# Performance work log

Measured on AMD Instinct MI355X. Metric: run time of the kernel, lower is better.

The kernel has to match this reference:

```python
import jax, jax.numpy as jnp
import numpy as np

BASIS_SIZE = 256          # levels of the bitfield code
R_MAX = 1.0               # quantization range for normalized weights
QMAX = BASIS_SIZE // 2 - 1  # 127 -> symmetric int8-style grid
EPS = 1e-8


def setup_inputs() -> dict:
    key = jax.random.key(0)
    kx, kw, kb = jax.random.split(key, 3)
    B, S, D_IN, D_OUT = 4, 2048, 4096, 4096
    x = jax.random.normal(kx, (B, S, D_IN), dtype=jnp.float32)
    W = jax.random.normal(kw, (D_OUT, D_IN), dtype=jnp.float32)
    bias = jax.random.normal(kb, (D_OUT,), dtype=jnp.float32)
    return {"x": x, "W": W, "bias": bias}


def _bitfield_dequant_weight(W):
    # per-output-row L2 norm (p=2, dim=1 in torch)
    weight_norms = jnp.sqrt(jnp.sum(W * W, axis=1))          # [out]
    W_normalized = W / (weight_norms[:, None] + EPS)          # rows ~unit norm
    # bitfield encode/decode: uniform symmetric quantization to BASIS_SIZE
    # levels in [-R_MAX, R_MAX]
    scale = R_MAX / QMAX
    Wq = jnp.round(jnp.clip(W_normalized, -R_MAX, R_MAX) / scale) * scale
    return Wq, weight_norms


def reference(x, W, bias):
    Wq, weight_norms = _bitfield_dequant_weight(W)
    B, S, D_IN = x.shape
    x2 = x.reshape(-1, D_IN)                                  # [B*S, in]
    # bitfield matmul on normalized weights
    out_norm = jnp.einsum('nd,od->no', x2, Wq)                # [B*S, out]
    # denormalize (restore row norms) + bias epilogue
    out = out_norm * weight_norms
    out = out.reshape(B, S, -1) + bias
    return out
```

## Files before the change

kernel.cpp:

```cpp
#include <hip/hip_runtime.h>

typedef __attribute__((ext_vector_type(4))) int i32x4;
typedef __attribute__((ext_vector_type(16))) int i32x16;
typedef unsigned long long ull;

#define D_IN  4096
#define D_OUT 4096
#define M_TOT 8192

__device__ __forceinline__ int pack4(float a, float b, float c, float d, float s) {
  int q0 = (int)rintf(a * s) & 255;
  int q1 = (int)rintf(b * s) & 255;
  int q2 = (int)rintf(c * s) & 255;
  int q3 = (int)rintf(d * s) & 255;
  return q0 | (q1 << 8) | (q2 << 16) | (q3 << 24);
}

__global__ void quant_pack_kernel(const float* __restrict__ x, const float* __restrict__ W,
                                  char* __restrict__ XP, char* __restrict__ WP,
                                  float* __restrict__ sx, float* __restrict__ sn) {
  __shared__ float  redf[4];
  __shared__ double redd[4];
  __shared__ float  bc;
  const int bid = blockIdx.x, t = threadIdx.x;

  if (bid < M_TOT) {
    const int r = bid;
    const float4* xr = (const float4*)(x + (size_t)r * D_IN);
    float4 v[4];
    float mx = 0.f;
#pragma unroll
    for (int q = 0; q < 4; q++) {
      v[q] = xr[t * 4 + q];
      mx = fmaxf(mx, fmaxf(fmaxf(fabsf(v[q].x), fabsf(v[q].y)),
                           fmaxf(fabsf(v[q].z), fabsf(v[q].w))));
    }
#pragma unroll
    for (int off = 32; off; off >>= 1) mx = fmaxf(mx, __shfl_xor(mx, off));
    if ((t & 63) == 0) redf[t >> 6] = mx;
    __syncthreads();
    if (t == 0) {
      float m = fmaxf(fmaxf(redf[0], redf[1]), fmaxf(redf[2], redf[3]));
      bc = m;
      sx[r] = m * (1.0f / 127.0f);
    }
    __syncthreads();
    const float inv = 127.0f / bc;
    int4 o;
    o.x = pack4(v[0].x, v[0].y, v[0].z, v[0].w, inv);
    o.y = pack4(v[1].x, v[1].y, v[1].z, v[1].w, inv);
    o.z = pack4(v[2].x, v[2].y, v[2].z, v[2].w, inv);
    o.w = pack4(v[3].x, v[3].y, v[3].z, v[3].w, inv);
    const size_t addr =
        ((size_t)((r >> 5) * 128 + (t >> 1)) * 64 + (t & 1) * 32 + (r & 31)) * 16;
    *(int4*)(XP + addr) = o;
  } else {
    const int r = bid - M_TOT;
    const float4* wr = (const float4*)(W + (size_t)r * D_IN);
    float4 v[4];
    double ss = 0.0;
#pragma unroll
    for (int q = 0; q < 4; q++) {
      v[q] = wr[t * 4 + q];
      ss += (double)v[q].x * v[q].x + (double)v[q].y * v[q].y +
            (double)v[q].z * v[q].z + (double)v[q].w * v[q].w;
    }
#pragma unroll
    for (int off = 32; off; off >>= 1) ss += __shfl_xor(ss, off);
    if ((t & 63) == 0) redd[t >> 6] = ss;
    __syncthreads();
    if (t == 0) {
      double tot = redd[0] + redd[1] + redd[2] + redd[3];
      float nrm = (float)sqrt(tot);
      bc = nrm;
      sn[r] = nrm * (1.0f / 127.0f);
    }
    __syncthreads();
    const float den = bc + 1e-8f;
    int4 o;
    int* op = (int*)&o;
#pragma unroll
    for (int q = 0; q < 4; q++) {
      float e[4] = {v[q].x, v[q].y, v[q].z, v[q].w};
      int qq[4];
#pragma unroll
      for (int c = 0; c < 4; c++) {
        float wn = e[c] / den;
        wn = fminf(1.0f, fmaxf(-1.0f, wn));
        qq[c] = (int)rintf(wn * 127.0f) & 255;
      }
      op[q] = qq[0] | (qq[1] << 8) | (qq[2] << 16) | (qq[3] << 24);
    }
    const size_t addr =
        ((size_t)((r >> 5) * 128 + (t >> 1)) * 64 + (t & 1) * 32 + (r & 31)) * 16;
    *(int4*)(WP + addr) = o;
  }
}


#define GLD(dst, p, off) \
  asm volatile("global_load_dwordx4 %0, %1, off offset:%2" : "=v"(dst) : "v"(p), "i"(off))

__device__ __forceinline__ void load16(ull (&pa)[4], ull (&pb)[4],
                                       i32x4 (&fa)[8], i32x4 (&fb)[8]) {
#pragma unroll
  for (int mi = 0; mi < 4; mi++) {
    GLD(fa[2 * mi],     pa[mi], 0);
    GLD(fa[2 * mi + 1], pa[mi], 1024);
    pa[mi] += 2048;
  }
#pragma unroll
  for (int ni = 0; ni < 4; ni++) {
    GLD(fb[2 * ni],     pb[ni], 0);
    GLD(fb[2 * ni + 1], pb[ni], 1024);
    pb[ni] += 2048;
  }
}

template<int VM>
__device__ __forceinline__ void mfma32(i32x4 (&fa)[8], i32x4 (&fb)[8],
                                       i32x16 (&acc)[4][4]) {
  asm volatile("s_waitcnt vmcnt(%[vm])"
               : "+v"(fa[0]), "+v"(fa[1]), "+v"(fa[2]), "+v"(fa[3]),
                 "+v"(fa[4]), "+v"(fa[5]), "+v"(fa[6]), "+v"(fa[7]),
                 "+v"(fb[0]), "+v"(fb[1]), "+v"(fb[2]), "+v"(fb[3]),
                 "+v"(fb[4]), "+v"(fb[5]), "+v"(fb[6]), "+v"(fb[7])
               : [vm] "i"(VM));
  __builtin_amdgcn_sched_barrier(0);
#pragma unroll
  for (int kk = 0; kk < 2; kk++)
#pragma unroll
    for (int mi = 0; mi < 4; mi++)
#pragma unroll
      for (int ni = 0; ni < 4; ni++)
        acc[mi][ni] = __builtin_amdgcn_mfma_i32_32x32x32_i8(
            fa[2 * mi + kk], fb[2 * ni + kk], acc[mi][ni], 0, 0, 0);
  __builtin_amdgcn_sched_barrier(0);
}

__global__ __launch_bounds__(256, 1)
void gemm_i8_kernel(const char* __restrict__ XP, const char* __restrict__ WP,
                    const float* __restrict__ sx, const float* __restrict__ sn,
                    const float* __restrict__ bias, float* __restrict__ C) {
  const int t = threadIdx.x;
  const int lane = t & 63;
  const int wave = t >> 6;
  const int wm = wave >> 1, wn = wave & 1;

  const int bid = blockIdx.x;
  const int xcd = bid & 7;
  const int j   = bid >> 3;
  const int nblk = xcd * 2 + (j & 1);
  const int mblk = j >> 1;
  const int m0 = mblk * 256, n0 = nblk * 256;

  const int mt0 = (m0 >> 5) + wm * 4;
  const int nt0 = (n0 >> 5) + wn * 4;
  ull pa[4], pb[4];
#pragma unroll
  for (int mi = 0; mi < 4; mi++)
    pa[mi] = (ull)(XP + (size_t)(mt0 + mi) * 131072 + lane * 16);
#pragma unroll
  for (int ni = 0; ni < 4; ni++)
    pb[ni] = (ull)(WP + (size_t)(nt0 + ni) * 131072 + lane * 16);

  i32x16 acc[4][4];
#pragma unroll
  for (int i = 0; i < 4; i++)
#pragma unroll
    for (int jj = 0; jj < 4; jj++) acc[i][jj] = (i32x16)0;
  i32x4 fAa[8], fAb[8], fBa[8], fBb[8];

  load16(pa, pb, fAa, fAb);
#pragma unroll 1
  for (int it = 0; it < 31; ++it) {
    load16(pa, pb, fBa, fBb);
    mfma32<16>(fAa, fAb, acc);
    load16(pa, pb, fAa, fAb);
    mfma32<16>(fBa, fBb, acc);
  }
  load16(pa, pb, fBa, fBb);
  mfma32<16>(fAa, fAb, acc);
  mfma32<0>(fBa, fBb, acc);

  const int l31 = lane & 31;
  const int hi  = lane >> 5;
#pragma unroll
  for (int mi = 0; mi < 4; mi++) {
    const int rbase = m0 + wm * 128 + mi * 32 + hi * 4;
    float sxv[16];
#pragma unroll
    for (int r = 0; r < 16; r++) sxv[r] = sx[rbase + (r & 3) + 8 * (r >> 2)];
#pragma unroll
    for (int ni = 0; ni < 4; ni++) {
      const int col = n0 + wn * 128 + ni * 32 + l31;
      const float scn = sn[col];
      const float bv  = bias[col];
#pragma unroll
      for (int r = 0; r < 16; r++) {
        const int row = rbase + (r & 3) + 8 * (r >> 2);
        C[(size_t)row * D_OUT + col] =
            (float)acc[mi][ni][r] * (sxv[r] * scn) + bv;
      }
    }
  }
}

extern "C" void kernel_launch(void* const* d_in, const int* in_sizes, int n_in,
                              void* d_out, int out_size, void* d_ws, size_t ws_size,
                              hipStream_t stream) {
  const float* x    = (const float*)d_in[0];
  const float* W    = (const float*)d_in[1];
  const float* bias = (const float*)d_in[2];
  float* out = (float*)d_out;

  char* ws = (char*)d_ws;
  char*  xp = ws;
  char*  wp = ws + (size_t)M_TOT * D_IN;
  float* sx = (float*)(wp + (size_t)D_OUT * D_IN);
  float* sn = sx + M_TOT;

  quant_pack_kernel<<<M_TOT + D_OUT, 256, 0, stream>>>(x, W, xp, wp, sx, sn);
  gemm_i8_kernel<<<512, 256, 0, stream>>>(xp, wp, sx, sn, bias, out);
}
```

Measured before the change: 400.2 us.

## Stage quantized tiles through LDS for coalesced stores and triple-buffer GEMM loads

```diff
diff --git a/kernel.cpp b/kernel.cpp
--- a/kernel.cpp
+++ b/kernel.cpp
@@ -8,92 +8,93 @@
 #define D_OUT 4096
 #define M_TOT 8192
 
-__device__ __forceinline__ int pack4(float a, float b, float c, float d, float s) {
-  int q0 = (int)rintf(a * s) & 255;
-  int q1 = (int)rintf(b * s) & 255;
-  int q2 = (int)rintf(c * s) & 255;
-  int q3 = (int)rintf(d * s) & 255;
-  return q0 | (q1 << 8) | (q2 << 16) | (q3 << 24);
-}
-
-__global__ void quant_pack_kernel(const float* __restrict__ x, const float* __restrict__ W,
-                                  char* __restrict__ XP, char* __restrict__ WP,
-                                  float* __restrict__ sx, float* __restrict__ sn) {
-  __shared__ float  redf[4];
-  __shared__ double redd[4];
-  __shared__ float  bc;
-  const int bid = blockIdx.x, t = threadIdx.x;
-
-  if (bid < M_TOT) {
-    const int r = bid;
-    const float4* xr = (const float4*)(x + (size_t)r * D_IN);
-    float4 v[4];
-    float mx = 0.f;
-#pragma unroll
-    for (int q = 0; q < 4; q++) {
-      v[q] = xr[t * 4 + q];
-      mx = fmaxf(mx, fmaxf(fmaxf(fabsf(v[q].x), fabsf(v[q].y)),
-                           fmaxf(fabsf(v[q].z), fabsf(v[q].w))));
+__global__ __launch_bounds__(512, 4)
+void quant_pack_kernel(const float* __restrict__ x, const float* __restrict__ W,
+                       char* __restrict__ XP, char* __restrict__ WP,
+                       float* __restrict__ sx, float* __restrict__ sn) {
+  __shared__ __align__(16) char img[65536];
+  const int bid  = blockIdx.x;
+  const int t    = threadIdx.x;
+  const int lane = t & 63;
+  const int wave = t >> 6;
+
+  const bool isX = bid < (M_TOT / 16);
+  const int  b2  = isX ? bid : bid - (M_TOT / 16);
+  const float* src = isX ? x : W;
+  char*  dst = isX ? XP : WP;
+  float* sc  = isX ? sx : sn;
+
+  const int g = lane >> 2, s4 = (lane & 3) << 2;
+
+#pragma unroll
+  for (int i = 0; i < 2; i++) {
+    const int rl = wave * 2 + i;
+    const int R  = b2 * 16 + rl;
+    const float4* xr4 = (const float4*)(src + (size_t)R * D_IN);
+
+    float4 v[16];
+#pragma unroll
+    for (int j = 0; j < 16; j++) v[j] = xr4[j * 64 + lane];
+
+    float inv;
+    if (isX) {
+      float mx = 0.f;
+#pragma unroll
+      for (int j = 0; j < 16; j++)
+        mx = fmaxf(mx, fmaxf(fmaxf(fabsf(v[j].x), fabsf(v[j].y)),
+                             fmaxf(fabsf(v[j].z), fabsf(v[j].w))));
+#pragma unroll
+      for (int off = 32; off; off >>= 1) mx = fmaxf(mx, __shfl_xor(mx, off));
+      if (lane == 0) sc[R] = mx * (1.0f / 127.0f);
+      inv = 127.0f / mx;
+      const unsigned wb = (unsigned)(g * 256 + ((rl ^ g) << 4) + s4);
+      int* ip = (int*)(img + wb);
+#pragma unroll
+      for (int j = 0; j < 16; j++) {
+        int q0 = (int)rintf(v[j].x * inv) & 255;
+        int q1 = (int)rintf(v[j].y * inv) & 255;
+        int q2 = (int)rintf(v[j].z * inv) & 255;
+        int q3 = (int)rintf(v[j].w * inv) & 255;
+        ip[j * 1024] = q0 | (q1 << 8) | (q2 << 16) | (q3 << 24);
+      }
+    } else {
+      double ss = 0.0;
+#pragma unroll
+      for (int j = 0; j < 16; j++)
+        ss += (double)v[j].x * v[j].x + (double)v[j].y * v[j].y +
+              (double)v[j].z * v[j].z + (double)v[j].w * v[j].w;
+#pragma unroll
+      for (int off = 32; off; off >>= 1) ss += __shfl_xor(ss, off);
+      const float nrm = (float)sqrt(ss);
+      if (lane == 0) sc[R] = nrm * (1.0f / 127.0f);
+      const float den = nrm + 1e-8f;
+      const unsigned wb = (unsigned)(g * 256 + ((rl ^ g) << 4) + s4);
+      int* ip = (int*)(img + wb);
+#pragma unroll
+      for (int j = 0; j < 16; j++) {
+        float e[4] = {v[j].x, v[j].y, v[j].z, v[j].w};
+        int q[4];
+#pragma unroll
+        for (int c = 0; c < 4; c++) {
+          float wn = e[c] / den;
+          wn = fminf(1.0f, fmaxf(-1.0f, wn));
+          q[c] = (int)rintf(wn * 127.0f) & 255;
+        }
+        ip[j * 1024] = q[0] | (q[1] << 8) | (q[2] << 16) | (q[3] << 24);
+      }
     }
-#pragma unroll
-    for (int off = 32; off; off >>= 1) mx = fmaxf(mx, __shfl_xor(mx, off));
-    if ((t & 63) == 0) redf[t >> 6] = mx;
-    __syncthreads();
-    if (t == 0) {
-      float m = fmaxf(fmaxf(redf[0], redf[1]), fmaxf(redf[2], redf[3]));
-      bc = m;
-      sx[r] = m * (1.0f / 127.0f);
-    }
-    __syncthreads();
-    const float inv = 127.0f / bc;
-    int4 o;
-    o.x = pack4(v[0].x, v[0].y, v[0].z, v[0].w, inv);
-    o.y = pack4(v[1].x, v[1].y, v[1].z, v[1].w, inv);
-    o.z = pack4(v[2].x, v[2].y, v[2].z, v[2].w, inv);
-    o.w = pack4(v[3].x, v[3].y, v[3].z, v[3].w, inv);
-    const size_t addr =
-        ((size_t)((r >> 5) * 128 + (t >> 1)) * 64 + (t & 1) * 32 + (r & 31)) * 16;
-    *(int4*)(XP + addr) = o;
-  } else {
-    const int r = bid - M_TOT;
-    const float4* wr = (const float4*)(W + (size_t)r * D_IN);
-    float4 v[4];
-    double ss = 0.0;
-#pragma unroll
-    for (int q = 0; q < 4; q++) {
-      v[q] = wr[t * 4 + q];
-      ss += (double)v[q].x * v[q].x + (double)v[q].y * v[q].y +
-            (double)v[q].z * v[q].z + (double)v[q].w * v[q].w;
-    }
-#pragma unroll
-    for (int off = 32; off; off >>= 1) ss += __shfl_xor(ss, off);
-    if ((t & 63) == 0) redd[t >> 6] = ss;
-    __syncthreads();
-    if (t == 0) {
-      double tot = redd[0] + redd[1] + redd[2] + redd[3];
-      float nrm = (float)sqrt(tot);
-      bc = nrm;
-      sn[r] = nrm * (1.0f / 127.0f);
-    }
-    __syncthreads();
-    const float den = bc + 1e-8f;
-    int4 o;
-    int* op = (int*)&o;
-#pragma unroll
-    for (int q = 0; q < 4; q++) {
-      float e[4] = {v[q].x, v[q].y, v[q].z, v[q].w};
-      int qq[4];
-#pragma unroll
-      for (int c = 0; c < 4; c++) {
-        float wn = e[c] / den;
-        wn = fminf(1.0f, fmaxf(-1.0f, wn));
-        qq[c] = (int)rintf(wn * 127.0f) & 255;
-      }
-      op[q] = qq[0] | (qq[1] << 8) | (qq[2] << 16) | (qq[3] << 24);
-    }
-    const size_t addr =
-        ((size_t)((r >> 5) * 128 + (t >> 1)) * 64 + (t & 1) * 32 + (r & 31)) * 16;
-    *(int4*)(WP + addr) = o;
+  }
+
+  __syncthreads();
+
+  char* gbase = dst + (size_t)(b2 >> 1) * 131072 + (b2 & 1) * 256;
+#pragma unroll
+  for (int i = 0; i < 8; i++) {
+    const int c  = t + 512 * i;
+    const int p  = c >> 4;
+    const int rl = c & 15;
+    int4 val = *(const int4*)(img + p * 256 + ((rl ^ (p & 15)) << 4));
+    *(int4*)(gbase + p * 512 + rl * 16) = val;
   }
 }
 
@@ -169,19 +170,25 @@
   for (int i = 0; i < 4; i++)
 #pragma unroll
     for (int jj = 0; jj < 4; jj++) acc[i][jj] = (i32x16)0;
-  i32x4 fAa[8], fAb[8], fBa[8], fBb[8];
+  i32x4 fAa[8], fAb[8], fBa[8], fBb[8], fCa[8], fCb[8];
 
   load16(pa, pb, fAa, fAb);
+  load16(pa, pb, fBa, fBb);
 #pragma unroll 1
-  for (int it = 0; it < 31; ++it) {
+  for (int it = 0; it < 20; ++it) {
+    load16(pa, pb, fCa, fCb);
+    mfma32<32>(fAa, fAb, acc);
+    load16(pa, pb, fAa, fAb);
+    mfma32<32>(fBa, fBb, acc);
     load16(pa, pb, fBa, fBb);
-    mfma32<16>(fAa, fAb, acc);
-    load16(pa, pb, fAa, fAb);
-    mfma32<16>(fBa, fBb, acc);
-  }
-  load16(pa, pb, fBa, fBb);
-  mfma32<16>(fAa, fAb, acc);
-  mfma32<0>(fBa, fBb, acc);
+    mfma32<32>(fCa, fCb, acc);
+  }
+  load16(pa, pb, fCa, fCb);
+  mfma32<32>(fAa, fAb, acc);
+  load16(pa, pb, fAa, fAb);
+  mfma32<32>(fBa, fBb, acc);
+  mfma32<16>(fCa, fCb, acc);
+  mfma32<0>(fAa, fAb, acc);
 
   const int l31 = lane & 31;
   const int hi  = lane >> 5;
@@ -220,6 +227,6 @@
   float* sx = (float*)(wp + (size_t)D_OUT * D_IN);
   float* sn = sx + M_TOT;
 
-  quant_pack_kernel<<<M_TOT + D_OUT, 256, 0, stream>>>(x, W, xp, wp, sx, sn);
+  quant_pack_kernel<<<(M_TOT + D_OUT) / 16, 512, 0, stream>>>(x, W, xp, wp, sx, sn);
   gemm_i8_kernel<<<512, 256, 0, stream>>>(xp, wp, sx, sn, bias, out);
 }
```

New measurement: 377.5 us. 1.06x faster.
